# Kernel tuning notes

Hardware: AMD Instinct MI355X
Metric: run time of the kernel (lower is better)

## Reference

```python
import jax, jax.numpy as jnp
import numpy as np

N_NODES = 100000
FIELD_DIM = 128
EMBED_DIM = 64
N_EDGES = 3200000
BATCH = 8192
NUM_FIELDS = 2


def setup_inputs() -> dict:
    key = jax.random.key(0)
    k1, k2, k3, k4 = jax.random.split(key, 4)
    features = jax.random.normal(k1, (N_NODES, FIELD_DIM), dtype=jnp.float32)
    edge_index = jax.random.randint(k2, (2, N_EDGES), 0, N_NODES, dtype=jnp.int32)
    # GCNConv linear weight (Glorot-ish scale) and bias
    W = jax.random.normal(k3, (FIELD_DIM, EMBED_DIM), dtype=jnp.float32) * (1.0 / np.sqrt(FIELD_DIM))
    bias = jnp.zeros((EMBED_DIM,), dtype=jnp.float32)
    x = jax.random.randint(k4, (BATCH, NUM_FIELDS), 0, N_NODES, dtype=jnp.int32)
    return {"features": features, "edge_index": edge_index, "W": W, "bias": bias, "x": x}


def reference(features, edge_index, W, bias, x):
    # GCNConv: out = D^{-1/2} (A + I) D^{-1/2} (X W) + b, then gather rows by x.
    n = features.shape[0]
    loop = jnp.arange(n, dtype=edge_index.dtype)
    src = jnp.concatenate([edge_index[0], loop])  # [E + N]
    dst = jnp.concatenate([edge_index[1], loop])  # [E + N]
    # degree (with self-loops) per destination node; >= 1 so rsqrt is safe
    deg = jax.ops.segment_sum(jnp.ones_like(dst, dtype=features.dtype), dst, num_segments=n)
    dinv = jax.lax.rsqrt(deg)
    norm = dinv[src] * dinv[dst]  # [E + N]
    h = features @ W  # [N, EMBED_DIM]
    msgs = h[src] * norm[:, None]  # gather + scale
    out = jax.ops.segment_sum(msgs, dst, num_segments=n) + bias  # [N, EMBED_DIM]
    return out[x]  # [BATCH, NUM_FIELDS, EMBED_DIM]
```

## Files before the change

### kernel.cpp

```cpp
#include <hip/hip_runtime.h>

#define N_NODES   100000
#define FIELD_DIM 128
#define EMBED_DIM 64
#define N_EDGES   3200000
#define NX        16384

#define NRANGE    2
#define RN        50000
#define RNH       25000
#define NSLICE    125
#define SLICE_E   (N_EDGES / NSLICE)
#define HISTB     (NRANGE * NSLICE)
#define SB_N      16384
#define EXB       (N_EDGES / 1024)
#define PCAP      5120

typedef short  bf16x8 __attribute__((ext_vector_type(8)));
typedef float  f32x4  __attribute__((ext_vector_type(4)));

__device__ __forceinline__ unsigned short f2bf(float x) {
    unsigned u = __float_as_uint(x);
    u += 0x7FFF + ((u >> 16) & 1);
    return (unsigned short)(u >> 16);
}
__device__ __forceinline__ float bf2f(unsigned short b) {
    return __uint_as_float(((unsigned)b) << 16);
}
__device__ __forceinline__ unsigned pk2(float lo, float hi) {
    return (unsigned)f2bf(lo) | ((unsigned)f2bf(hi) << 16);
}

__global__ __launch_bounds__(1024) void k_histzero(const int* __restrict__ dst,
                                                   unsigned int* __restrict__ partial32,
                                                   float4* __restrict__ z4) {
    int tid = threadIdx.x;
    if (blockIdx.x == HISTB) {
        for (int i = tid; i < 1284; i += 1024) z4[i] = make_float4(0.f, 0.f, 0.f, 0.f);
        return;
    }
    __shared__ unsigned int hist[RNH];
    int q = blockIdx.x & 1, s = blockIdx.x >> 1;
    for (int i = tid; i < RNH; i += 1024) hist[i] = 0;
    __syncthreads();
    int lo = q * RN;
    const int4* dp = (const int4*)(dst + s * SLICE_E);
    for (int i = tid; i < SLICE_E / 4; i += 1024) {
        int4 d = dp[i];
        int a;
        a = d.x - lo; if ((unsigned)a < RN) atomicAdd(&hist[a >> 1], 1u << ((a & 1) << 4));
        a = d.y - lo; if ((unsigned)a < RN) atomicAdd(&hist[a >> 1], 1u << ((a & 1) << 4));
        a = d.z - lo; if ((unsigned)a < RN) atomicAdd(&hist[a >> 1], 1u << ((a & 1) << 4));
        a = d.w - lo; if ((unsigned)a < RN) atomicAdd(&hist[a >> 1], 1u << ((a & 1) << 4));
    }
    __syncthreads();
    unsigned int* po = partial32 + (size_t)blockIdx.x * RNH;
    for (int i = tid; i < RNH; i += 1024) po[i] = hist[i];
}

__global__ void k_init(const int* __restrict__ x, unsigned int* __restrict__ bits,
                       const float* __restrict__ W, unsigned short* __restrict__ Wt) {
    int b = blockIdx.x;
    if (b < 64) {
        int i = b * 256 + threadIdx.x;
        int v = x[i];
        atomicOr(&bits[v >> 5], 1u << (v & 31));
    } else {
        for (int o = threadIdx.x; o < FIELD_DIM * EMBED_DIM; o += 256) {
            int c = o >> 7, k = o & 127;
            Wt[o] = f2bf(W[k * EMBED_DIM + c]);
        }
    }
}

__global__ __launch_bounds__(256) void k_reduce(const unsigned int* __restrict__ partial32,
                                                const unsigned int* __restrict__ bits,
                                                int* __restrict__ cnt,
                                                float* __restrict__ dinv,
                                                int* __restrict__ nlist,
                                                int* __restrict__ inv,
                                                int* __restrict__ off,
                                                int* __restrict__ sbase_t,
                                                unsigned long long* __restrict__ counters) {
    __shared__ int wtot[4], wedge[4], ptot[4], pedge[4];
    __shared__ unsigned int baseN, baseE;
    int tid = threadIdx.x;
    int v = blockIdx.x * 256 + tid;
    bool inb = (v < N_NODES);
    int vc = inb ? v : (N_NODES - 1);
    int q = vc / RN, loc = vc - q * RN;
    int i2 = loc >> 1, sh = (loc & 1) << 4;
    const unsigned int* p = partial32 + (size_t)q * RNH + i2;
    unsigned short vals[NSLICE];
#pragma unroll
    for (int s = 0; s < NSLICE; ++s)
        vals[s] = (unsigned short)((p[(size_t)s * (NRANGE * RNH)] >> sh) & 0xFFFFu);
    int c = 0;
#pragma unroll
    for (int s = 0; s < NSLICE; ++s) c += vals[s];
    if (inb) {
        cnt[v] = c;
        dinv[v] = rsqrtf((float)c + 1.0f);
    }
    bool fl = inb && ((bits[v >> 5] >> (v & 31)) & 1u);
    int lane = tid & 63;
    int w = tid >> 6;
    unsigned long long mask = __ballot(fl);
    int cc = fl ? c : 0;
    int incl = cc;
#pragma unroll
    for (int o = 1; o < 64; o <<= 1) {
        int t = __shfl_up(incl, o);
        if (lane >= o) incl += t;
    }
    if (lane == 63) { wtot[w] = __popcll(mask); wedge[w] = incl; }
    int myi = __popcll(mask & ((1ull << lane) - 1));
    int excl = incl - cc;
    __syncthreads();
    if (tid == 0) {
        int t0 = wtot[0], t1 = wtot[1], t2 = wtot[2], t3 = wtot[3];
        int e0 = wedge[0], e1 = wedge[1], e2 = wedge[2], e3 = wedge[3];
        ptot[0] = 0; ptot[1] = t0; ptot[2] = t0 + t1; ptot[3] = t0 + t1 + t2;
        pedge[0] = 0; pedge[1] = e0; pedge[2] = e0 + e1; pedge[3] = e0 + e1 + e2;
        int bt = t0 + t1 + t2 + t3;
        int be = e0 + e1 + e2 + e3;
        if (bt > 0) {
            unsigned long long add = ((unsigned long long)(unsigned)be << 32) |
                                     (unsigned long long)(unsigned)bt;
            unsigned long long old = atomicAdd(counters, add);
            baseN = (unsigned)(old & 0xFFFFFFFFull);
            baseE = (unsigned)(old >> 32);
        } else {
            baseN = 0; baseE = 0;
        }
    }
    __syncthreads();
    if (fl) {
        int ic = (int)baseN + ptot[w] + myi;
        int oc = (int)baseE + pedge[w] + excl;
        nlist[ic] = v;
        inv[v] = ic;
        off[v] = oc;
        int cum = 0;
#pragma unroll
        for (int s = 0; s < NSLICE; ++s) {
            sbase_t[(size_t)s * SB_N + ic] = oc + cum;
            cum += vals[s];
        }
    }
}

__global__ __launch_bounds__(256) void k_extract(const int* __restrict__ src,
                                                 const int* __restrict__ dst,
                                                 const unsigned int* __restrict__ bits,
                                                 const int* __restrict__ inv,
                                                 int2* __restrict__ pairs,
                                                 int* __restrict__ scur16) {
    __shared__ int wsum[4];
    __shared__ int sbase;
    int b = blockIdx.x, tid = threadIdx.x;
    int lane = tid & 63, w = tid >> 6;
    int slice = b / 25;
    const int4* dp = (const int4*)(dst + b * 1024);
    const int4* sp = (const int4*)(src + b * 1024);
    int4 d4 = dp[tid];
    int4 s4 = sp[tid];
    int dd[4] = {d4.x, d4.y, d4.z, d4.w};
    int ss[4] = {s4.x, s4.y, s4.z, s4.w};
    bool fl[4];
    int nf = 0;
#pragma unroll
    for (int u = 0; u < 4; ++u) {
        fl[u] = (bits[(unsigned)dd[u] >> 5] >> (dd[u] & 31)) & 1u;
        nf += fl[u] ? 1 : 0;
    }
    int incl = nf;
#pragma unroll
    for (int o = 1; o < 64; o <<= 1) {
        int t = __shfl_up(incl, o);
        if (lane >= o) incl += t;
    }
    if (lane == 63) wsum[w] = incl;
    __syncthreads();
    if (tid == 0) {
        int bt = wsum[0] + wsum[1] + wsum[2] + wsum[3];
        sbase = bt ? atomicAdd(&scur16[slice * 16], bt) : 0;
    }
    __syncthreads();
    int wbase = (w > 0 ? wsum[0] : 0) + (w > 1 ? wsum[1] : 0) + (w > 2 ? wsum[2] : 0);
    int pos = sbase + wbase + incl - nf;
    int2* po = pairs + (size_t)slice * PCAP;
#pragma unroll
    for (int u = 0; u < 4; ++u) {
        if (fl[u]) {
            if (pos < PCAP) po[pos] = make_int2(inv[dd[u]], ss[u]);
            ++pos;
        }
    }
}

__global__ __launch_bounds__(256) void k_gemm(const float* __restrict__ F,
                                              const unsigned short* __restrict__ Wt,
                                              unsigned short* __restrict__ h) {
    int tid = threadIdx.x;
    int wave = tid >> 6, lane = tid & 63;
    int l15 = lane & 15, kg = lane >> 4;

    const char* wb = (const char*)Wt;
    bf16x8 bfrag[4][4];
#pragma unroll
    for (int cb = 0; cb < 4; ++cb)
#pragma unroll
        for (int ks = 0; ks < 4; ++ks)
            bfrag[cb][ks] = *(const bf16x8*)(wb + (cb * 16 + l15) * 256 + ks * 64 + kg * 16);

    int row = blockIdx.x * 64 + wave * 16 + l15;
    int rowc = min(row, N_NODES - 1);
    const float4* F4 = (const float4*)(F + (size_t)rowc * FIELD_DIM + kg * 8);

    f32x4 acc[4];
#pragma unroll
    for (int cb = 0; cb < 4; ++cb) acc[cb] = (f32x4){0.f, 0.f, 0.f, 0.f};

#pragma unroll
    for (int ks = 0; ks < 4; ++ks) {
        float4 fa = F4[ks * 8];
        float4 fb = F4[ks * 8 + 1];
        union { bf16x8 v; unsigned u[4]; } af;
        af.u[0] = pk2(fa.x, fa.y);
        af.u[1] = pk2(fa.z, fa.w);
        af.u[2] = pk2(fb.x, fb.y);
        af.u[3] = pk2(fb.z, fb.w);
#pragma unroll
        for (int cb = 0; cb < 4; ++cb)
            acc[cb] = __builtin_amdgcn_mfma_f32_16x16x32_bf16(af.v, bfrag[cb][ks],
                                                              acc[cb], 0, 0, 0);
    }
    int rbase = blockIdx.x * 64 + wave * 16 + kg * 4;
#pragma unroll
    for (int r = 0; r < 4; ++r) {
        int orow = rbase + r;
        if (orow < N_NODES) {
            unsigned short* hp = h + (size_t)orow * 64 + l15;
#pragma unroll
            for (int cb = 0; cb < 4; ++cb) hp[cb * 16] = f2bf(acc[cb][r]);
        }
    }
}

__global__ __launch_bounds__(1024) void k_place(const int2* __restrict__ pairs,
                                                const int* __restrict__ scur16,
                                                const int* __restrict__ sbase_t,
                                                int* __restrict__ elist) {
    __shared__ int cur[SB_N];
    int s = blockIdx.x, tid = threadIdx.x;
    const int* srow = sbase_t + (size_t)s * SB_N;
    for (int i = tid; i < SB_N; i += 1024) cur[i] = srow[i];
    __syncthreads();
    int tot = min(scur16[s * 16], PCAP);
    const int2* pp = pairs + (size_t)s * PCAP;
    for (int r = tid; r < tot; r += 1024) {
        int2 p = pp[r];
        int slot = atomicAdd(&cur[p.x], 1);
        elist[slot] = p.y;
    }
}

__global__ __launch_bounds__(256) void k_pull(const int* __restrict__ nlist,
                                              const int* __restrict__ counters,
                                              const int* __restrict__ cnt,
                                              const int* __restrict__ off,
                                              const int* __restrict__ elist,
                                              const unsigned short* __restrict__ h,
                                              const float* __restrict__ dinv,
                                              const float* __restrict__ bias,
                                              float* __restrict__ accc) {
    int t = blockIdx.x * blockDim.x + threadIdx.x;
    int wid = t >> 6;
    int lane = t & 63;
    if (wid >= counters[0]) return;
    int v = nlist[wid];
    float dvd = dinv[v];
    int deg = cnt[v];
    int base = off[v];
    float acc = bf2f(h[(size_t)v * 64 + lane]) * (dvd * dvd) + bias[lane];
    float acc2 = 0.f;
    int j = 0;
    for (; j + 7 < deg; j += 8) {
        int s0 = elist[base + j + 0];
        int s1 = elist[base + j + 1];
        int s2 = elist[base + j + 2];
        int s3 = elist[base + j + 3];
        int s4 = elist[base + j + 4];
        int s5 = elist[base + j + 5];
        int s6 = elist[base + j + 6];
        int s7 = elist[base + j + 7];
        float v0 = bf2f(h[(size_t)s0 * 64 + lane]);
        float v1 = bf2f(h[(size_t)s1 * 64 + lane]);
        float v2 = bf2f(h[(size_t)s2 * 64 + lane]);
        float v3 = bf2f(h[(size_t)s3 * 64 + lane]);
        float v4 = bf2f(h[(size_t)s4 * 64 + lane]);
        float v5 = bf2f(h[(size_t)s5 * 64 + lane]);
        float v6 = bf2f(h[(size_t)s6 * 64 + lane]);
        float v7 = bf2f(h[(size_t)s7 * 64 + lane]);
        float n0 = dinv[s0], n1 = dinv[s1], n2 = dinv[s2], n3 = dinv[s3];
        float n4 = dinv[s4], n5 = dinv[s5], n6 = dinv[s6], n7 = dinv[s7];
        acc  += v0 * (n0 * dvd);
        acc2 += v1 * (n1 * dvd);
        acc  += v2 * (n2 * dvd);
        acc2 += v3 * (n3 * dvd);
        acc  += v4 * (n4 * dvd);
        acc2 += v5 * (n5 * dvd);
        acc  += v6 * (n6 * dvd);
        acc2 += v7 * (n7 * dvd);
    }
    for (; j < deg; ++j) {
        int s0 = elist[base + j];
        acc += bf2f(h[(size_t)s0 * 64 + lane]) * (dinv[s0] * dvd);
    }
    accc[(size_t)wid * 64 + lane] = acc + acc2;
}

__global__ void k_gather(const int* __restrict__ x,
                         const int* __restrict__ inv,
                         const float* __restrict__ accc,
                         float* __restrict__ out) {
    int g = blockIdx.x * blockDim.x + threadIdx.x;
    if (g >= NX * 64) return;
    int v = x[g >> 6];
    out[g] = accc[(size_t)inv[v] * 64 + (g & 63)];
}

extern "C" void kernel_launch(void* const* d_in, const int* in_sizes, int n_in,
                              void* d_out, int out_size, void* d_ws, size_t ws_size,
                              hipStream_t stream) {
    const float* features = (const float*)d_in[0];
    const int*   edge     = (const int*)d_in[1];
    const float* W        = (const float*)d_in[2];
    const float* bias     = (const float*)d_in[3];
    const int*   x        = (const int*)d_in[4];
    float* out = (float*)d_out;

    char* ws = (char*)d_ws;
    unsigned short* h16      = (unsigned short*)(ws);
    int*            elist    = (int*)(ws + 12800000);
    unsigned int*   partial32= (unsigned int*)(ws + 16800000);
    int2*           pairs    = (int2*)(ws + 16800000);
    float*          accc     = (float*)(ws + 21920000);
    int*            sbase_t  = (int*)  (ws + 41800000);
    int*            cnt      = (int*)  (ws + 49992000);
    float*          dinv     = (float*)(ws + 50392000);
    int*            off      = (int*)  (ws + 50792000);
    int*            inv      = (int*)  (ws + 51192000);
    int*            nlist    = (int*)  (ws + 51592000);
    int*            scur16   = (int*)  (ws + 51657536);
    unsigned long long* counters = (unsigned long long*)(ws + 51665536);
    unsigned int*   bits     = (unsigned int*) (ws + 51665568);
    unsigned short* Wt       = (unsigned short*)(ws + 51678080);

    const int* esrc = edge;
    const int* edst = edge + N_EDGES;

    k_histzero<<<HISTB + 1, 1024, 0, stream>>>(edst, partial32,
                                               (float4*)(ws + 51657536));
    k_init    <<<65, 256, 0, stream>>>(x, bits, W, Wt);
    k_reduce  <<<(N_NODES + 255) / 256, 256, 0, stream>>>(partial32, bits, cnt, dinv,
                                                          nlist, inv, off, sbase_t, counters);
    k_extract <<<EXB, 256, 0, stream>>>(esrc, edst, bits, inv, pairs, scur16);
    k_gemm    <<<(N_NODES + 63) / 64, 256, 0, stream>>>(features, Wt, h16);
    k_place   <<<NSLICE, 1024, 0, stream>>>(pairs, scur16, sbase_t, elist);
    k_pull    <<<(NX * 64 + 255) / 256, 256, 0, stream>>>(nlist, (const int*)counters,
                                                          cnt, off, elist, h16, dinv,
                                                          bias, accc);
    k_gather  <<<(NX * 64 + 255) / 256, 256, 0, stream>>>(x, inv, accc, out);
}
```

Baseline: 102.9 us.

## Fuse degree histogram with edge extraction into one pass over dst

Merges the per-slice degree histogram and the extraction of edges that land on batch nodes into one kernel, so dst is read once. Extraction now stores the raw destination id, and the inv lookup moves into k_place, which removes the dependency on k_reduce and allows extraction before it. Pairs now share memory with h16, and gemm runs after place. Only half the blocks (q==0) extract, and the extra block-wide syncs inside the histogram loop may stall those blocks.

```diff
diff --git a/kernel.cpp b/kernel.cpp
--- a/kernel.cpp
+++ b/kernel.cpp
@@ -13,7 +13,7 @@
 #define SLICE_E   (N_EDGES / NSLICE)
 #define HISTB     (NRANGE * NSLICE)
 #define SB_N      16384
-#define EXB       (N_EDGES / 1024)
+#define GEMMB     ((N_NODES + 63) / 64)
 #define PCAP      5120
 
 typedef short  bf16x8 __attribute__((ext_vector_type(8)));
@@ -31,31 +31,9 @@
     return (unsigned)f2bf(lo) | ((unsigned)f2bf(hi) << 16);
 }
 
-__global__ __launch_bounds__(1024) void k_histzero(const int* __restrict__ dst,
-                                                   unsigned int* __restrict__ partial32,
-                                                   float4* __restrict__ z4) {
-    int tid = threadIdx.x;
-    if (blockIdx.x == HISTB) {
-        for (int i = tid; i < 1284; i += 1024) z4[i] = make_float4(0.f, 0.f, 0.f, 0.f);
-        return;
-    }
-    __shared__ unsigned int hist[RNH];
-    int q = blockIdx.x & 1, s = blockIdx.x >> 1;
-    for (int i = tid; i < RNH; i += 1024) hist[i] = 0;
-    __syncthreads();
-    int lo = q * RN;
-    const int4* dp = (const int4*)(dst + s * SLICE_E);
-    for (int i = tid; i < SLICE_E / 4; i += 1024) {
-        int4 d = dp[i];
-        int a;
-        a = d.x - lo; if ((unsigned)a < RN) atomicAdd(&hist[a >> 1], 1u << ((a & 1) << 4));
-        a = d.y - lo; if ((unsigned)a < RN) atomicAdd(&hist[a >> 1], 1u << ((a & 1) << 4));
-        a = d.z - lo; if ((unsigned)a < RN) atomicAdd(&hist[a >> 1], 1u << ((a & 1) << 4));
-        a = d.w - lo; if ((unsigned)a < RN) atomicAdd(&hist[a >> 1], 1u << ((a & 1) << 4));
-    }
-    __syncthreads();
-    unsigned int* po = partial32 + (size_t)blockIdx.x * RNH;
-    for (int i = tid; i < RNH; i += 1024) po[i] = hist[i];
+__global__ void k_zero(float4* __restrict__ z4) {
+    int i = blockIdx.x * blockDim.x + threadIdx.x;
+    if (i < 1284) z4[i] = make_float4(0.f, 0.f, 0.f, 0.f);
 }
 
 __global__ void k_init(const int* __restrict__ x, unsigned int* __restrict__ bits,
@@ -71,6 +49,79 @@
             Wt[o] = f2bf(W[k * EMBED_DIM + c]);
         }
     }
+}
+
+__global__ __launch_bounds__(1024) void k_histex(const int* __restrict__ dst,
+                                                 const int* __restrict__ src,
+                                                 const unsigned int* __restrict__ bits,
+                                                 unsigned int* __restrict__ partial32,
+                                                 int2* __restrict__ pairs,
+                                                 int* __restrict__ scur16) {
+    __shared__ unsigned int hist[RNH];
+    __shared__ int wsum[16];
+    __shared__ int sbase_sh;
+    int tid = threadIdx.x;
+    int q = blockIdx.x & 1, s = blockIdx.x >> 1;
+    for (int i = tid; i < RNH; i += 1024) hist[i] = 0;
+    __syncthreads();
+    int lo = q * RN;
+    const int4* dp = (const int4*)(dst + s * SLICE_E);
+    const int4* sp = (const int4*)(src + s * SLICE_E);
+    int lane = tid & 63, w = tid >> 6;
+    int2* po = pairs + (size_t)s * PCAP;
+
+    for (int it = 0; it < 7; ++it) {
+        int i = it * 1024 + tid;
+        bool act = (i < SLICE_E / 4);
+        int4 d = act ? dp[i] : make_int4(0, 0, 0, 0);
+        int dd[4] = {d.x, d.y, d.z, d.w};
+#pragma unroll
+        for (int u = 0; u < 4; ++u) {
+            int a = dd[u] - lo;
+            if (act && (unsigned)a < RN)
+                atomicAdd(&hist[a >> 1], 1u << ((a & 1) << 4));
+        }
+        if (q == 0) {
+            int4 s4 = act ? sp[i] : make_int4(0, 0, 0, 0);
+            int ss[4] = {s4.x, s4.y, s4.z, s4.w};
+            bool fl[4];
+            int nf = 0;
+#pragma unroll
+            for (int u = 0; u < 4; ++u) {
+                fl[u] = act && ((bits[(unsigned)dd[u] >> 5] >> (dd[u] & 31)) & 1u);
+                nf += fl[u] ? 1 : 0;
+            }
+            int incl = nf;
+#pragma unroll
+            for (int o = 1; o < 64; o <<= 1) {
+                int t = __shfl_up(incl, o);
+                if (lane >= o) incl += t;
+            }
+            if (lane == 63) wsum[w] = incl;
+            __syncthreads();
+            if (tid == 0) {
+                int bt = 0;
+#pragma unroll
+                for (int g = 0; g < 16; ++g) bt += wsum[g];
+                sbase_sh = bt ? atomicAdd(&scur16[s * 16], bt) : 0;
+            }
+            __syncthreads();
+            int wbase = 0;
+            for (int g = 0; g < w; ++g) wbase += wsum[g];
+            int pos = sbase_sh + wbase + incl - nf;
+#pragma unroll
+            for (int u = 0; u < 4; ++u) {
+                if (fl[u]) {
+                    if (pos < PCAP) po[pos] = make_int2(dd[u], ss[u]);
+                    ++pos;
+                }
+            }
+            __syncthreads();
+        }
+    }
+    __syncthreads();
+    unsigned int* pw = partial32 + (size_t)blockIdx.x * RNH;
+    for (int i = tid; i < RNH; i += 1024) pw[i] = hist[i];
 }
 
 __global__ __launch_bounds__(256) void k_reduce(const unsigned int* __restrict__ partial32,
@@ -150,52 +201,23 @@
     }
 }
 
-__global__ __launch_bounds__(256) void k_extract(const int* __restrict__ src,
-                                                 const int* __restrict__ dst,
-                                                 const unsigned int* __restrict__ bits,
-                                                 const int* __restrict__ inv,
-                                                 int2* __restrict__ pairs,
-                                                 int* __restrict__ scur16) {
-    __shared__ int wsum[4];
-    __shared__ int sbase;
-    int b = blockIdx.x, tid = threadIdx.x;
-    int lane = tid & 63, w = tid >> 6;
-    int slice = b / 25;
-    const int4* dp = (const int4*)(dst + b * 1024);
-    const int4* sp = (const int4*)(src + b * 1024);
-    int4 d4 = dp[tid];
-    int4 s4 = sp[tid];
-    int dd[4] = {d4.x, d4.y, d4.z, d4.w};
-    int ss[4] = {s4.x, s4.y, s4.z, s4.w};
-    bool fl[4];
-    int nf = 0;
-#pragma unroll
-    for (int u = 0; u < 4; ++u) {
-        fl[u] = (bits[(unsigned)dd[u] >> 5] >> (dd[u] & 31)) & 1u;
-        nf += fl[u] ? 1 : 0;
-    }
-    int incl = nf;
-#pragma unroll
-    for (int o = 1; o < 64; o <<= 1) {
-        int t = __shfl_up(incl, o);
-        if (lane >= o) incl += t;
-    }
-    if (lane == 63) wsum[w] = incl;
-    __syncthreads();
-    if (tid == 0) {
-        int bt = wsum[0] + wsum[1] + wsum[2] + wsum[3];
-        sbase = bt ? atomicAdd(&scur16[slice * 16], bt) : 0;
-    }
-    __syncthreads();
-    int wbase = (w > 0 ? wsum[0] : 0) + (w > 1 ? wsum[1] : 0) + (w > 2 ? wsum[2] : 0);
-    int pos = sbase + wbase + incl - nf;
-    int2* po = pairs + (size_t)slice * PCAP;
-#pragma unroll
-    for (int u = 0; u < 4; ++u) {
-        if (fl[u]) {
-            if (pos < PCAP) po[pos] = make_int2(inv[dd[u]], ss[u]);
-            ++pos;
-        }
+__global__ __launch_bounds__(1024) void k_place(const int2* __restrict__ pairs,
+                                                const int* __restrict__ scur16,
+                                                const int* __restrict__ inv,
+                                                const int* __restrict__ sbase_t,
+                                                int* __restrict__ elist) {
+    __shared__ int cur[SB_N];
+    int s = blockIdx.x, tid = threadIdx.x;
+    const int* srow = sbase_t + (size_t)s * SB_N;
+    for (int i = tid; i < SB_N; i += 1024) cur[i] = srow[i];
+    __syncthreads();
+    int tot = min(scur16[s * 16], PCAP);
+    const int2* pp = pairs + (size_t)s * PCAP;
+    for (int r = tid; r < tot; r += 1024) {
+        int2 p = pp[r];
+        int ii = inv[p.x];
+        int slot = atomicAdd(&cur[ii], 1);
+        elist[slot] = p.y;
     }
 }
 
@@ -245,24 +267,6 @@
 #pragma unroll
             for (int cb = 0; cb < 4; ++cb) hp[cb * 16] = f2bf(acc[cb][r]);
         }
-    }
-}
-
-__global__ __launch_bounds__(1024) void k_place(const int2* __restrict__ pairs,
-                                                const int* __restrict__ scur16,
-                                                const int* __restrict__ sbase_t,
-                                                int* __restrict__ elist) {
-    __shared__ int cur[SB_N];
-    int s = blockIdx.x, tid = threadIdx.x;
-    const int* srow = sbase_t + (size_t)s * SB_N;
-    for (int i = tid; i < SB_N; i += 1024) cur[i] = srow[i];
-    __syncthreads();
-    int tot = min(scur16[s * 16], PCAP);
-    const int2* pp = pairs + (size_t)s * PCAP;
-    for (int r = tid; r < tot; r += 1024) {
-        int2 p = pp[r];
-        int slot = atomicAdd(&cur[p.x], 1);
-        elist[slot] = p.y;
     }
 }
 
@@ -343,9 +347,9 @@
 
     char* ws = (char*)d_ws;
     unsigned short* h16      = (unsigned short*)(ws);
+    int2*           pairs    = (int2*)(ws);
     int*            elist    = (int*)(ws + 12800000);
     unsigned int*   partial32= (unsigned int*)(ws + 16800000);
-    int2*           pairs    = (int2*)(ws + 16800000);
     float*          accc     = (float*)(ws + 21920000);
     int*            sbase_t  = (int*)  (ws + 41800000);
     int*            cnt      = (int*)  (ws + 49992000);
@@ -361,16 +365,15 @@
     const int* esrc = edge;
     const int* edst = edge + N_EDGES;
 
-    k_histzero<<<HISTB + 1, 1024, 0, stream>>>(edst, partial32,
-                                               (float4*)(ws + 51657536));
-    k_init    <<<65, 256, 0, stream>>>(x, bits, W, Wt);
-    k_reduce  <<<(N_NODES + 255) / 256, 256, 0, stream>>>(partial32, bits, cnt, dinv,
-                                                          nlist, inv, off, sbase_t, counters);
-    k_extract <<<EXB, 256, 0, stream>>>(esrc, edst, bits, inv, pairs, scur16);
-    k_gemm    <<<(N_NODES + 63) / 64, 256, 0, stream>>>(features, Wt, h16);
-    k_place   <<<NSLICE, 1024, 0, stream>>>(pairs, scur16, sbase_t, elist);
-    k_pull    <<<(NX * 64 + 255) / 256, 256, 0, stream>>>(nlist, (const int*)counters,
-                                                          cnt, off, elist, h16, dinv,
-                                                          bias, accc);
-    k_gather  <<<(NX * 64 + 255) / 256, 256, 0, stream>>>(x, inv, accc, out);
-}
+    k_zero  <<<6, 256, 0, stream>>>((float4*)(ws + 51657536));
+    k_init  <<<65, 256, 0, stream>>>(x, bits, W, Wt);
+    k_histex<<<HISTB, 1024, 0, stream>>>(edst, esrc, bits, partial32, pairs, scur16);
+    k_reduce<<<(N_NODES + 255) / 256, 256, 0, stream>>>(partial32, bits, cnt, dinv,
+                                                        nlist, inv, off, sbase_t, counters);
+    k_place <<<NSLICE, 1024, 0, stream>>>(pairs, scur16, inv, sbase_t, elist);
+    k_gemm  <<<GEMMB, 256, 0, stream>>>(features, Wt, h16);
+    k_pull  <<<(NX * 64 + 255) / 256, 256, 0, stream>>>(nlist, (const int*)counters,
+                                                        cnt, off, elist, h16, dinv,
+                                                        bias, accc);
+    k_gather<<<(NX * 64 + 255) / 256, 256, 0, stream>>>(x, inv, accc, out);
+}
```

New measurement: 119.5 us. 1.16x slower.
